# Performance work log

Hardware: AMD Instinct MI355X
Metric: run time of the kernel (lower is better)

## Reference

```python
import jax, jax.numpy as jnp
import numpy as np

N = 1_000_000          # atoms
D_IN = 118             # one-hot atom-type dim
D_OUT = 64             # embedded feature dim
NUM_SEG = 4096         # graphs in batch


def setup_inputs() -> dict:
    key = jax.random.key(0)
    k1, k2, k3, k4 = jax.random.split(key, 4)
    x = jax.random.normal(k1, (N, D_IN), dtype=jnp.float32)
    W = jax.random.normal(k2, (D_OUT, D_IN), dtype=jnp.float32) * (1.0 / np.sqrt(D_IN))
    b = jax.random.normal(k3, (D_OUT,), dtype=jnp.float32) * 0.01
    batch = jnp.sort(jax.random.randint(k4, (N,), 0, NUM_SEG, dtype=jnp.int64))
    return {"x": x, "W": W, "b": b, "batch": batch, "num_segments": NUM_SEG}


def reference(x, W, b, batch, num_segments):
    # linear + relu (per-atom embedding)
    h = jax.nn.relu(jnp.einsum("nd,od->no", x, W) + b)  # [N, D_OUT]
    # opaque inner model treated as identity
    # scatter_add over graph ids (segment reduce)
    s = jax.ops.segment_sum(h, batch, num_segments=num_segments)  # [G, D_OUT]
    s = jax.nn.relu(s)
    # max-normalize each graph's feature vector
    maxima = jnp.max(s, axis=1, keepdims=True)  # [G, 1]
    return s / maxima
```

## Files before the change

### kernel.cpp

```cpp
#include <hip/hip_runtime.h>
#include <hip/hip_bf16.h>
#include <stdint.h>

#define D_IN 118
#define D_OUT 64
#define KPAD 128
#define BM 128
#define XS_STRIDE 136

typedef __attribute__((ext_vector_type(8))) short bf16x8;
typedef __attribute__((ext_vector_type(4))) float floatx4;

__device__ __forceinline__ uint16_t f2bf(float f) {
    uint32_t u;
    __builtin_memcpy(&u, &f, 4);
    uint32_t r = (u + 0x7fffu + ((u >> 16) & 1u)) >> 16;
    return (uint16_t)r;
}

__device__ __forceinline__ uint32_t pack_bf16(float a, float b) {
    return (uint32_t)f2bf(a) | ((uint32_t)f2bf(b) << 16);
}

__global__ void wconv(const float* __restrict__ W, ushort* __restrict__ Wt) {
    int idx = blockIdx.x * 256 + threadIdx.x;
    if (idx >= D_OUT * KPAD) return;
    int o = idx >> 7, k = idx & 127;
    float v = (k < D_IN) ? W[o * D_IN + k] : 0.f;
    Wt[idx] = f2bf(v);
}

__global__ __launch_bounds__(256) void fused_main(
    const float* __restrict__ x, const ushort* __restrict__ Wt,
    const float* __restrict__ bias, const int* __restrict__ batch,
    float* __restrict__ out, int n_atoms)
{
    __shared__ __align__(16) ushort xs[BM * XS_STRIDE];
    __shared__ int ids[BM];

    const int tid = threadIdx.x;
    const int atom0 = blockIdx.x * BM;

    if (tid < BM) {
        int a = atom0 + tid;
        ids[tid] = (a < n_atoms) ? batch[a] : -1;
    }

#pragma unroll
    for (int ph = 0; ph < 8; ++ph) {
        int tau = ph * 256 + tid;
        int m = tau >> 4, c = tau & 15;
        long row = atom0 + m;
        bool rok = row < n_atoms;
        const float* src = x + row * D_IN + c * 8;
        uint32_t pk[4];
#pragma unroll
        for (int j = 0; j < 4; ++j) {
            int k = c * 8 + j * 2;
            float2 v = make_float2(0.f, 0.f);
            if (rok && k < D_IN) v = *reinterpret_cast<const float2*>(src + j * 2);
            pk[j] = pack_bf16(v.x, v.y);
        }
        *reinterpret_cast<uint4*>(&xs[m * XS_STRIDE + c * 8]) =
            make_uint4(pk[0], pk[1], pk[2], pk[3]);
    }

    const int lane = tid & 63;
    const int wv = tid >> 6;
    const int n = lane & 15;
    const int q = lane >> 4;

    bf16x8 bfrag[4][4];
#pragma unroll
    for (int ot = 0; ot < 4; ++ot)
#pragma unroll
        for (int ks = 0; ks < 4; ++ks) {
            const ushort* p = Wt + (ot * 16 + n) * KPAD + ks * 32 + q * 8;
            bfrag[ot][ks] = *reinterpret_cast<const bf16x8*>(p);
        }

    __syncthreads();

    floatx4 acc[2][4];
#pragma unroll
    for (int mt = 0; mt < 2; ++mt)
#pragma unroll
        for (int ot = 0; ot < 4; ++ot)
            acc[mt][ot] = (floatx4){0.f, 0.f, 0.f, 0.f};

#pragma unroll
    for (int ks = 0; ks < 4; ++ks) {
        bf16x8 afrag[2];
#pragma unroll
        for (int mt = 0; mt < 2; ++mt) {
            int row = wv * 32 + mt * 16 + n;
            afrag[mt] = *reinterpret_cast<const bf16x8*>(
                &xs[row * XS_STRIDE + ks * 32 + q * 8]);
        }
#pragma unroll
        for (int mt = 0; mt < 2; ++mt)
#pragma unroll
            for (int ot = 0; ot < 4; ++ot)
                acc[mt][ot] = __builtin_amdgcn_mfma_f32_16x16x32_bf16(
                    afrag[mt], bfrag[ot][ks], acc[mt][ot], 0, 0, 0);
    }

    float bv[4];
#pragma unroll
    for (int ot = 0; ot < 4; ++ot) bv[ot] = bias[ot * 16 + n];

    float racc[4] = {0.f, 0.f, 0.f, 0.f};
    int cur = ids[wv * 32 + q * 4];
#pragma unroll
    for (int mt = 0; mt < 2; ++mt) {
#pragma unroll
        for (int reg = 0; reg < 4; ++reg) {
            int r = wv * 32 + mt * 16 + q * 4 + reg;
            int id = ids[r];
            if (id != cur) {
                if (cur >= 0) {
#pragma unroll
                    for (int ot = 0; ot < 4; ++ot)
                        atomicAdd(&out[cur * 64 + ot * 16 + n], racc[ot]);
                }
                cur = id;
                racc[0] = racc[1] = racc[2] = racc[3] = 0.f;
            }
#pragma unroll
            for (int ot = 0; ot < 4; ++ot) {
                float h = acc[mt][ot][reg] + bv[ot];
                racc[ot] += fmaxf(h, 0.f);
            }
        }
    }
    if (cur >= 0) {
#pragma unroll
        for (int ot = 0; ot < 4; ++ot)
            atomicAdd(&out[cur * 64 + ot * 16 + n], racc[ot]);
    }
}

__global__ void finalize(float* __restrict__ out, int nseg) {
    int row = blockIdx.x * 4 + (threadIdx.x >> 6);
    int lane = threadIdx.x & 63;
    if (row >= nseg) return;
    float v = fmaxf(out[row * 64 + lane], 0.f);
    float m = v;
#pragma unroll
    for (int off = 32; off > 0; off >>= 1)
        m = fmaxf(m, __shfl_xor(m, off, 64));
    out[row * 64 + lane] = v / m;
}

extern "C" void kernel_launch(void* const* d_in, const int* in_sizes, int n_in,
                              void* d_out, int out_size, void* d_ws, size_t ws_size,
                              hipStream_t stream) {
    const float* x = (const float*)d_in[0];
    const float* W = (const float*)d_in[1];
    const float* b = (const float*)d_in[2];
    const int* batch = (const int*)d_in[3];
    int n_atoms = in_sizes[0] / D_IN;
    int nseg = out_size / D_OUT;
    float* out = (float*)d_out;
    ushort* Wt = (ushort*)d_ws;

    hipMemsetAsync(d_out, 0, (size_t)out_size * sizeof(float), stream);
    wconv<<<dim3((D_OUT * KPAD + 255) / 256), dim3(256), 0, stream>>>(W, Wt);
    int nblocks = (n_atoms + BM - 1) / BM;
    fused_main<<<dim3(nblocks), dim3(256), 0, stream>>>(x, Wt, b, batch, out, n_atoms);
    finalize<<<dim3((nseg + 3) / 4), dim3(256), 0, stream>>>(out, nseg);
}
```

Before: 696.7 us.

## Pre-reduce segment sums in shared memory and load x directly into MFMA fragments

Each block now covers 64 atoms. Every wave loads its x rows straight from global memory into bf16 MFMA A-fragments, so the shared-memory staging tile and its barrier are gone. Per-lane partial segment sums go to a small shared-memory table indexed relative to the block's first segment id, using LDS atomics. Each block then flushes only the nonzero entries to global memory. This cuts the heavy contention of many global atomics hitting the same segment addresses. The cost is less coalesced global loads (16 rows per wave, 32-byte chunks), a serialized k-loop, and a fallback to global atomics when a block spans more than 16 segments.

```diff
diff --git a/kernel.cpp b/kernel.cpp
--- a/kernel.cpp
+++ b/kernel.cpp
@@ -5,8 +5,7 @@
 #define D_IN 118
 #define D_OUT 64
 #define KPAD 128
-#define BM 128
-#define XS_STRIDE 136
+#define MAXSEG 16
 
 typedef __attribute__((ext_vector_type(8))) short bf16x8;
 typedef __attribute__((ext_vector_type(4))) float floatx4;
@@ -14,8 +13,7 @@
 __device__ __forceinline__ uint16_t f2bf(float f) {
     uint32_t u;
     __builtin_memcpy(&u, &f, 4);
-    uint32_t r = (u + 0x7fffu + ((u >> 16) & 1u)) >> 16;
-    return (uint16_t)r;
+    return (uint16_t)((u + 0x7fffu + ((u >> 16) & 1u)) >> 16);
 }
 
 __device__ __forceinline__ uint32_t pack_bf16(float a, float b) {
@@ -35,108 +33,115 @@
     const float* __restrict__ bias, const int* __restrict__ batch,
     float* __restrict__ out, int n_atoms)
 {
-    __shared__ __align__(16) ushort xs[BM * XS_STRIDE];
-    __shared__ int ids[BM];
+    __shared__ float segacc[MAXSEG * 64];
 
     const int tid = threadIdx.x;
-    const int atom0 = blockIdx.x * BM;
-
-    if (tid < BM) {
-        int a = atom0 + tid;
-        ids[tid] = (a < n_atoms) ? batch[a] : -1;
-    }
-
-#pragma unroll
-    for (int ph = 0; ph < 8; ++ph) {
-        int tau = ph * 256 + tid;
-        int m = tau >> 4, c = tau & 15;
-        long row = atom0 + m;
-        bool rok = row < n_atoms;
-        const float* src = x + row * D_IN + c * 8;
-        uint32_t pk[4];
-#pragma unroll
-        for (int j = 0; j < 4; ++j) {
-            int k = c * 8 + j * 2;
-            float2 v = make_float2(0.f, 0.f);
-            if (rok && k < D_IN) v = *reinterpret_cast<const float2*>(src + j * 2);
-            pk[j] = pack_bf16(v.x, v.y);
-        }
-        *reinterpret_cast<uint4*>(&xs[m * XS_STRIDE + c * 8]) =
-            make_uint4(pk[0], pk[1], pk[2], pk[3]);
-    }
-
     const int lane = tid & 63;
     const int wv = tid >> 6;
     const int n = lane & 15;
     const int q = lane >> 4;
 
-    bf16x8 bfrag[4][4];
 #pragma unroll
-    for (int ot = 0; ot < 4; ++ot)
-#pragma unroll
-        for (int ks = 0; ks < 4; ++ks) {
-            const ushort* p = Wt + (ot * 16 + n) * KPAD + ks * 32 + q * 8;
-            bfrag[ot][ks] = *reinterpret_cast<const bf16x8*>(p);
-        }
-
+    for (int i = 0; i < (MAXSEG * 64) / 256; ++i)
+        segacc[i * 256 + tid] = 0.0f;
     __syncthreads();
 
-    floatx4 acc[2][4];
+    const int rowbase = blockIdx.x * 64 + wv * 16;
+    const int myrow = rowbase + n;
+    const bool rok = myrow < n_atoms;
+    const float* __restrict__ arow = x + (long)myrow * D_IN;
+
+    floatx4 acc[4];
 #pragma unroll
-    for (int mt = 0; mt < 2; ++mt)
+    for (int ot = 0; ot < 4; ++ot) acc[ot] = (floatx4){0.f, 0.f, 0.f, 0.f};
+
+#pragma unroll 1
+    for (int ks = 0; ks < 4; ++ks) {
+        const int k0 = ks * 32 + q * 8;
+        uint32_t pk[4];
 #pragma unroll
-        for (int ot = 0; ot < 4; ++ot)
-            acc[mt][ot] = (floatx4){0.f, 0.f, 0.f, 0.f};
+        for (int j2 = 0; j2 < 4; ++j2) {
+            int k = k0 + j2 * 2;
+            float2 v = make_float2(0.f, 0.f);
+            if (rok && k + 1 < D_IN)
+                v = *reinterpret_cast<const float2*>(arow + k);
+            pk[j2] = pack_bf16(v.x, v.y);
+        }
+        bf16x8 afrag;
+        __builtin_memcpy(&afrag, pk, 16);
 
 #pragma unroll
-    for (int ks = 0; ks < 4; ++ks) {
-        bf16x8 afrag[2];
-#pragma unroll
-        for (int mt = 0; mt < 2; ++mt) {
-            int row = wv * 32 + mt * 16 + n;
-            afrag[mt] = *reinterpret_cast<const bf16x8*>(
-                &xs[row * XS_STRIDE + ks * 32 + q * 8]);
+        for (int ot = 0; ot < 4; ++ot) {
+            bf16x8 bfrag = *reinterpret_cast<const bf16x8*>(
+                Wt + (ot * 16 + n) * KPAD + k0);
+            acc[ot] = __builtin_amdgcn_mfma_f32_16x16x32_bf16(
+                afrag, bfrag, acc[ot], 0, 0, 0);
         }
-#pragma unroll
-        for (int mt = 0; mt < 2; ++mt)
-#pragma unroll
-            for (int ot = 0; ot < 4; ++ot)
-                acc[mt][ot] = __builtin_amdgcn_mfma_f32_16x16x32_bf16(
-                    afrag[mt], bfrag[ot][ks], acc[mt][ot], 0, 0, 0);
     }
 
     float bv[4];
 #pragma unroll
     for (int ot = 0; ot < 4; ++ot) bv[ot] = bias[ot * 16 + n];
 
+    int idr = rowbase + q * 4;
+    int4 myids = make_int4(-1, -1, -1, -1);
+    if (idr + 3 < n_atoms) {
+        myids = *reinterpret_cast<const int4*>(batch + idr);
+    } else if (idr < n_atoms) {
+        const int* bp = batch + idr;
+        myids.x = bp[0];
+        if (idr + 1 < n_atoms) myids.y = bp[1];
+        if (idr + 2 < n_atoms) myids.z = bp[2];
+    }
+    int ids4[4] = {myids.x, myids.y, myids.z, myids.w};
+
+    const int s_first = batch[blockIdx.x * 64];
+
     float racc[4] = {0.f, 0.f, 0.f, 0.f};
-    int cur = ids[wv * 32 + q * 4];
+    int cur = ids4[0];
 #pragma unroll
-    for (int mt = 0; mt < 2; ++mt) {
+    for (int reg = 0; reg < 4; ++reg) {
+        int id = ids4[reg];
+        if (id != cur) {
+            if (cur >= 0) {
+                int si = cur - s_first;
+                if (si < MAXSEG) {
 #pragma unroll
-        for (int reg = 0; reg < 4; ++reg) {
-            int r = wv * 32 + mt * 16 + q * 4 + reg;
-            int id = ids[r];
-            if (id != cur) {
-                if (cur >= 0) {
+                    for (int ot = 0; ot < 4; ++ot)
+                        atomicAdd(&segacc[si * 64 + ot * 16 + n], racc[ot]);
+                } else {
 #pragma unroll
                     for (int ot = 0; ot < 4; ++ot)
                         atomicAdd(&out[cur * 64 + ot * 16 + n], racc[ot]);
                 }
-                cur = id;
-                racc[0] = racc[1] = racc[2] = racc[3] = 0.f;
             }
+            cur = id;
+            racc[0] = racc[1] = racc[2] = racc[3] = 0.f;
+        }
 #pragma unroll
-            for (int ot = 0; ot < 4; ++ot) {
-                float h = acc[mt][ot][reg] + bv[ot];
-                racc[ot] += fmaxf(h, 0.f);
-            }
+        for (int ot = 0; ot < 4; ++ot)
+            racc[ot] += fmaxf(acc[ot][reg] + bv[ot], 0.f);
+    }
+    if (cur >= 0) {
+        int si = cur - s_first;
+        if (si < MAXSEG) {
+#pragma unroll
+            for (int ot = 0; ot < 4; ++ot)
+                atomicAdd(&segacc[si * 64 + ot * 16 + n], racc[ot]);
+        } else {
+#pragma unroll
+            for (int ot = 0; ot < 4; ++ot)
+                atomicAdd(&out[cur * 64 + ot * 16 + n], racc[ot]);
         }
     }
-    if (cur >= 0) {
+
+    __syncthreads();
 #pragma unroll
-        for (int ot = 0; ot < 4; ++ot)
-            atomicAdd(&out[cur * 64 + ot * 16 + n], racc[ot]);
+    for (int i0 = 0; i0 < (MAXSEG * 64) / 256; ++i0) {
+        int i = i0 * 256 + tid;
+        float v = segacc[i];
+        if (v != 0.0f)
+            atomicAdd(&out[(s_first + (i >> 6)) * 64 + (i & 63)], v);
     }
 }
 
@@ -166,7 +171,7 @@
 
     hipMemsetAsync(d_out, 0, (size_t)out_size * sizeof(float), stream);
     wconv<<<dim3((D_OUT * KPAD + 255) / 256), dim3(256), 0, stream>>>(W, Wt);
-    int nblocks = (n_atoms + BM - 1) / BM;
+    int nblocks = (n_atoms + 63) / 64;
     fused_main<<<dim3(nblocks), dim3(256), 0, stream>>>(x, Wt, b, batch, out, n_atoms);
     finalize<<<dim3((nseg + 3) / 4), dim3(256), 0, stream>>>(out, nseg);
 }
```

Result: slower. 722.8 us (+3.7%).
